# Optimization experiments

Measured on AMD Instinct MI355X. Metric: run time of the kernel, lower is better.

## Reference

```python
import jax, jax.numpy as jnp
import numpy as np

N_SRC = 50000
N_DST = 50000
N_EDGES = 600000
IN_FEAT = 128
OUT_FEAT = 128


def setup_inputs() -> dict:
    key = jax.random.key(0)
    k1, k2, k3, k4, k5, k6 = jax.random.split(key, 6)
    h_s = jax.random.normal(k1, (N_SRC, IN_FEAT), dtype=jnp.float32)
    h_d = jax.random.normal(k2, (N_DST, IN_FEAT), dtype=jnp.float32)
    src = jax.random.randint(k3, (N_EDGES,), 0, N_SRC, dtype=jnp.int32)
    dst = jax.random.randint(k4, (N_EDGES,), 0, N_DST, dtype=jnp.int32)
    # nn.Linear(in_feat*2, out_feat): W [out, 2*in], b [out]
    W = jax.random.normal(k5, (OUT_FEAT, 2 * IN_FEAT), dtype=jnp.float32) * 0.05
    b = jax.random.normal(k6, (OUT_FEAT,), dtype=jnp.float32) * 0.05
    return {"h_s": h_s, "h_d": h_d, "src": src, "dst": dst, "W": W, "b": b}


def reference(h_s, h_d, src, dst, W, b):
    # copy_u + mean: gather source features along edges, segment-mean by dst
    msgs = h_s[src]  # [E, in_feat]
    neigh_sum = jax.ops.segment_sum(msgs, dst, num_segments=N_DST)  # [n_dst, in_feat]
    deg = jax.ops.segment_sum(jnp.ones((src.shape[0],), dtype=h_s.dtype), dst,
                              num_segments=N_DST)
    h_neigh = neigh_sum / jnp.maximum(deg, 1.0)[:, None]  # zero-degree -> 0
    # concat + linear (dropout is identity in eval mode)
    feat = jnp.concatenate([h_d, h_neigh], axis=1)  # [n_dst, 2*in_feat]
    out = feat @ W.T + b  # [n_dst, out_feat]
    return out
```

## Files before the change

### kernel.cpp

```cpp
#include <hip/hip_runtime.h>
#include <hip/hip_bf16.h>

#define N_SRC 50000
#define N_DST 50000
#define N_EDGES 600000
#define IN_FEAT 128
#define OUT_FEAT 128
#define CAP 64

typedef __attribute__((ext_vector_type(8))) short short8;
typedef __attribute__((ext_vector_type(4))) float float4v;
typedef __attribute__((ext_vector_type(4))) float f32x4;

#define FILL_BLOCKS ((N_EDGES + 255) / 256)
#define HS4 (N_SRC * IN_FEAT / 4)
#define CVT_BLOCKS (HS4 / 256)
#define W_BLOCKS 16
#define K1_GRID (FILL_BLOCKS + 2 * CVT_BLOCKS + W_BLOCKS)

__global__ __launch_bounds__(256) void fill_cvt_kernel(
    const float* __restrict__ h_s, const float* __restrict__ h_d,
    const float* __restrict__ W,
    const int* __restrict__ src, const int* __restrict__ dst,
    int* __restrict__ deg, ushort* __restrict__ permu,
    ushort* __restrict__ hsb, ushort* __restrict__ hdb,
    ushort* __restrict__ wfrag)
{
    int bid = blockIdx.x;
    int tid = threadIdx.x;

    if (bid < FILL_BLOCKS) {
        int e = bid * 256 + tid;
        if (e < N_EDGES) {
            int s = __builtin_nontemporal_load(src + e);
            int d = __builtin_nontemporal_load(dst + e);
            int p = atomicAdd(&deg[d], 1);
            if (p < CAP) permu[(size_t)d * CAP + p] = (ushort)s;
        }
        return;
    }
    bid -= FILL_BLOCKS;

    if (bid < 2 * CVT_BLOCKS) {
        bool first = (bid < CVT_BLOCKS);
        const float* in = first ? h_s : h_d;
        ushort* outp    = first ? hsb : hdb;
        int idx = (first ? bid : bid - CVT_BLOCKS) * 256 + tid;
        f32x4 v = __builtin_nontemporal_load((const f32x4*)in + idx);
        __hip_bfloat16 o[4];
        o[0] = __float2bfloat16(v.x);
        o[1] = __float2bfloat16(v.y);
        o[2] = __float2bfloat16(v.z);
        o[3] = __float2bfloat16(v.w);
        *(ushort4*)(outp + (size_t)idx * 4) = *(ushort4*)o;
        return;
    }
    bid -= 2 * CVT_BLOCKS;

    int c = bid * 256 + tid;
    int f  = c >> 6;
    int l  = c & 63;
    int ks = f >> 3;
    int nt = f & 7;
    int row = nt * 16 + (l & 15);
    int col = ks * 32 + (l >> 4) * 8;
    const float* wp = W + (size_t)row * 256 + col;
    f32x4 w0 = __builtin_nontemporal_load((const f32x4*)wp);
    f32x4 w1 = __builtin_nontemporal_load((const f32x4*)wp + 1);
    __hip_bfloat16 o[8];
    o[0] = __float2bfloat16(w0.x); o[1] = __float2bfloat16(w0.y);
    o[2] = __float2bfloat16(w0.z); o[3] = __float2bfloat16(w0.w);
    o[4] = __float2bfloat16(w1.x); o[5] = __float2bfloat16(w1.y);
    o[6] = __float2bfloat16(w1.z); o[7] = __float2bfloat16(w1.w);
    *(short8*)(wfrag + (size_t)c * 8) = *(short8*)o;
}

__global__ __launch_bounds__(256) void gather_kernel(
    const ushort* __restrict__ hsb, const int* __restrict__ deg,
    const ushort* __restrict__ permu, ushort* __restrict__ neighb)
{
    int wave = threadIdx.x >> 6;
    int lane = threadIdx.x & 63;
    int row  = blockIdx.x * 4 + wave;
    if (row >= N_DST) return;

    int dg  = deg[row];
    int dgr = (dg < CAP) ? dg : CAP;
    const ushort* prow = permu + (size_t)row * CAP;
    int s0 = (dgr > 0) ? (int)prow[0] : 0;

    float ax = 0.f, ay = 0.f;
    for (int j = 0; j < dgr; j += 8) {
        ushort4 pa = *(const ushort4*)(prow + j);
        ushort4 pb = *(const ushort4*)(prow + j + 4);
        int t[8] = {pa.x, pa.y, pa.z, pa.w, pb.x, pb.y, pb.z, pb.w};
        int   s[8];
        float m[8];
#pragma unroll
        for (int q = 0; q < 8; ++q) {
            bool ok = (j + q < dgr);
            s[q] = ok ? t[q] : s0;
            m[q] = ok ? 1.f : 0.f;
        }
        ushort2 u[8];
#pragma unroll
        for (int q = 0; q < 8; ++q)
            u[q] = ((const ushort2*)(hsb + (size_t)s[q] * IN_FEAT))[lane];
#pragma unroll
        for (int q = 0; q < 8; ++q) {
            ax += m[q] * __uint_as_float((unsigned)u[q].x << 16);
            ay += m[q] * __uint_as_float((unsigned)u[q].y << 16);
        }
    }
    float inv = (dg > 0) ? (1.0f / (float)dg) : 0.0f;
    __hip_bfloat16 ox = __float2bfloat16(ax * inv);
    __hip_bfloat16 oy = __float2bfloat16(ay * inv);
    ushort2 o = make_ushort2(*(ushort*)&ox, *(ushort*)&oy);
    ((ushort2*)(neighb + (size_t)row * IN_FEAT))[lane] = o;
}

__global__ __launch_bounds__(256) void gemm_mfma_kernel(
    const ushort* __restrict__ hdb, const ushort* __restrict__ neighb,
    const ushort* __restrict__ wfrag, const float* __restrict__ b,
    float* __restrict__ out)
{
    __shared__ ushort sWb[64 * 64 * 8];

    int tid  = threadIdx.x;
    int wave = tid >> 6;
    int lane = tid & 63;
    int lm   = lane & 15;
    int lk   = (lane >> 4) * 8;

#pragma unroll
    for (int i = 0; i < 16; ++i) {
        int c = i * 256 + tid;
        *(short8*)(sWb + (size_t)c * 8) = *(const short8*)(wfrag + (size_t)c * 8);
    }
    __syncthreads();

    int row0 = blockIdx.x * 128 + wave * 32;

    float4v acc0[8], acc1[8];
#pragma unroll
    for (int nt = 0; nt < 8; ++nt) {
        acc0[nt] = (float4v){0.f, 0.f, 0.f, 0.f};
        acc1[nt] = (float4v){0.f, 0.f, 0.f, 0.f};
    }

    int ar0 = row0 + lm;       ar0 = (ar0 < N_DST) ? ar0 : (N_DST - 1);
    int ar1 = row0 + 16 + lm;  ar1 = (ar1 < N_DST) ? ar1 : (N_DST - 1);
    const ushort* a0h = hdb    + (size_t)ar0 * IN_FEAT + lk;
    const ushort* a1h = hdb    + (size_t)ar1 * IN_FEAT + lk;
    const ushort* a0n = neighb + (size_t)ar0 * IN_FEAT + lk;
    const ushort* a1n = neighb + (size_t)ar1 * IN_FEAT + lk;

#pragma unroll
    for (int ks = 0; ks < 8; ++ks) {
        int koff = (ks & 3) * 32;
        short8 af0 = (ks < 4) ? *(const short8*)(a0h + koff)
                              : *(const short8*)(a0n + koff);
        short8 af1 = (ks < 4) ? *(const short8*)(a1h + koff)
                              : *(const short8*)(a1n + koff);
#pragma unroll
        for (int nt = 0; nt < 8; ++nt) {
            short8 bf = *(const short8*)(sWb + ((size_t)(ks * 8 + nt) * 64 + lane) * 8);
            acc0[nt] = __builtin_amdgcn_mfma_f32_16x16x32_bf16(af0, bf, acc0[nt], 0, 0, 0);
            acc1[nt] = __builtin_amdgcn_mfma_f32_16x16x32_bf16(af1, bf, acc1[nt], 0, 0, 0);
        }
    }

    int orow0 = row0 + (lane >> 4) * 4;
#pragma unroll
    for (int nt = 0; nt < 8; ++nt) {
        int col = nt * 16 + lm;
        float bias = b[col];
#pragma unroll
        for (int r = 0; r < 4; ++r) {
            int oa = orow0 + r;
            int ob = oa + 16;
            if (oa < N_DST) out[(size_t)oa * OUT_FEAT + col] = acc0[nt][r] + bias;
            if (ob < N_DST) out[(size_t)ob * OUT_FEAT + col] = acc1[nt][r] + bias;
        }
    }
}

extern "C" void kernel_launch(void* const* d_in, const int* in_sizes, int n_in,
                              void* d_out, int out_size, void* d_ws, size_t ws_size,
                              hipStream_t stream) {
    const float* h_s = (const float*)d_in[0];
    const float* h_d = (const float*)d_in[1];
    const int*   src = (const int*)d_in[2];
    const int*   dst = (const int*)d_in[3];
    const float* W   = (const float*)d_in[4];
    const float* b   = (const float*)d_in[5];
    float* out = (float*)d_out;

    char* ws = (char*)d_ws;
    int*    deg    = (int*)ws;
    ushort* permu  = (ushort*)(ws + 200000);
    ushort* hsb    = (ushort*)(ws + 6600000);
    ushort* hdb    = (ushort*)(ws + 19400000);
    ushort* neighb = (ushort*)(ws + 32200000);
    ushort* wfrag  = (ushort*)(ws + 45000000);

    hipMemsetAsync(deg, 0, N_DST * sizeof(int), stream);

    fill_cvt_kernel<<<K1_GRID, 256, 0, stream>>>(
        h_s, h_d, W, src, dst, deg, permu, hsb, hdb, wfrag);
    gather_kernel<<<(N_DST + 3) / 4, 256, 0, stream>>>(
        hsb, deg, permu, neighb);
    gemm_mfma_kernel<<<(N_DST + 127) / 128, 256, 0, stream>>>(
        hdb, neighb, wfrag, b, out);
}
```

Measured before the change: 180.0 us.

## Add nontemporal stores, unroll first gather batch, drop LDS staging in GEMM

Conversion, gather and GEMM outputs now use nontemporal stores, and GEMM activations use nontemporal loads. The gather kernel issues the first 16 neighbour loads unconditionally, with out-of-range entries pointing at row 0 and masked to zero, which exposes more memory-level parallelism for typical degrees. The GEMM drops its per-block shared-memory copy of W and reads fragments straight from global/L2. It also halves rows per wave, doubling the grid so more blocks run concurrently. In exchange, the GEMM does more redundant W reads from cache, and nontemporal stores may evict data the next kernel wants to reuse.

Result: no change. 178.8 us (-0.6%).

```diff
diff --git a/kernel.cpp b/kernel.cpp
--- a/kernel.cpp
+++ b/kernel.cpp
@@ -11,6 +11,7 @@
 typedef __attribute__((ext_vector_type(8))) short short8;
 typedef __attribute__((ext_vector_type(4))) float float4v;
 typedef __attribute__((ext_vector_type(4))) float f32x4;
+typedef __attribute__((ext_vector_type(4))) unsigned short ushort4v;
 
 #define FILL_BLOCKS ((N_EDGES + 255) / 256)
 #define HS4 (N_SRC * IN_FEAT / 4)
@@ -52,7 +53,7 @@
         o[1] = __float2bfloat16(v.y);
         o[2] = __float2bfloat16(v.z);
         o[3] = __float2bfloat16(v.w);
-        *(ushort4*)(outp + (size_t)idx * 4) = *(ushort4*)o;
+        __builtin_nontemporal_store(*(ushort4v*)o, (ushort4v*)(outp + (size_t)idx * 4));
         return;
     }
     bid -= 2 * CVT_BLOCKS;
@@ -72,7 +73,7 @@
     o[2] = __float2bfloat16(w0.z); o[3] = __float2bfloat16(w0.w);
     o[4] = __float2bfloat16(w1.x); o[5] = __float2bfloat16(w1.y);
     o[6] = __float2bfloat16(w1.z); o[7] = __float2bfloat16(w1.w);
-    *(short8*)(wfrag + (size_t)c * 8) = *(short8*)o;
+    __builtin_nontemporal_store(*(short8*)o, (short8*)(wfrag + (size_t)c * 8));
 }
 
 __global__ __launch_bounds__(256) void gather_kernel(
@@ -87,36 +88,50 @@
     int dg  = deg[row];
     int dgr = (dg < CAP) ? dg : CAP;
     const ushort* prow = permu + (size_t)row * CAP;
-    int s0 = (dgr > 0) ? (int)prow[0] : 0;
 
     float ax = 0.f, ay = 0.f;
-    for (int j = 0; j < dgr; j += 8) {
+    {
+        ushort4 p0 = *(const ushort4*)(prow);
+        ushort4 p1 = *(const ushort4*)(prow + 4);
+        ushort4 p2 = *(const ushort4*)(prow + 8);
+        ushort4 p3 = *(const ushort4*)(prow + 12);
+        int t[16] = {p0.x, p0.y, p0.z, p0.w, p1.x, p1.y, p1.z, p1.w,
+                     p2.x, p2.y, p2.z, p2.w, p3.x, p3.y, p3.z, p3.w};
+        ushort2 u[16];
+#pragma unroll
+        for (int q = 0; q < 16; ++q) {
+            int s = (q < dgr) ? t[q] : 0;
+            u[q] = ((const ushort2*)(hsb + (size_t)s * IN_FEAT))[lane];
+        }
+#pragma unroll
+        for (int q = 0; q < 16; ++q) {
+            float m = (q < dgr) ? 1.f : 0.f;
+            ax += m * __uint_as_float((unsigned)u[q].x << 16);
+            ay += m * __uint_as_float((unsigned)u[q].y << 16);
+        }
+    }
+    for (int j = 16; j < dgr; j += 8) {
         ushort4 pa = *(const ushort4*)(prow + j);
         ushort4 pb = *(const ushort4*)(prow + j + 4);
         int t[8] = {pa.x, pa.y, pa.z, pa.w, pb.x, pb.y, pb.z, pb.w};
-        int   s[8];
-        float m[8];
+        ushort2 u[8];
 #pragma unroll
         for (int q = 0; q < 8; ++q) {
-            bool ok = (j + q < dgr);
-            s[q] = ok ? t[q] : s0;
-            m[q] = ok ? 1.f : 0.f;
-        }
-        ushort2 u[8];
-#pragma unroll
-        for (int q = 0; q < 8; ++q)
-            u[q] = ((const ushort2*)(hsb + (size_t)s[q] * IN_FEAT))[lane];
+            int s = (j + q < dgr) ? t[q] : 0;
+            u[q] = ((const ushort2*)(hsb + (size_t)s * IN_FEAT))[lane];
+        }
 #pragma unroll
         for (int q = 0; q < 8; ++q) {
-            ax += m[q] * __uint_as_float((unsigned)u[q].x << 16);
-            ay += m[q] * __uint_as_float((unsigned)u[q].y << 16);
+            float m = (j + q < dgr) ? 1.f : 0.f;
+            ax += m * __uint_as_float((unsigned)u[q].x << 16);
+            ay += m * __uint_as_float((unsigned)u[q].y << 16);
         }
     }
     float inv = (dg > 0) ? (1.0f / (float)dg) : 0.0f;
     __hip_bfloat16 ox = __float2bfloat16(ax * inv);
     __hip_bfloat16 oy = __float2bfloat16(ay * inv);
-    ushort2 o = make_ushort2(*(ushort*)&ox, *(ushort*)&oy);
-    ((ushort2*)(neighb + (size_t)row * IN_FEAT))[lane] = o;
+    unsigned pk = (unsigned)*(ushort*)&ox | ((unsigned)*(ushort*)&oy << 16);
+    __builtin_nontemporal_store(pk, (unsigned*)(neighb + (size_t)row * IN_FEAT) + lane);
 }
 
 __global__ __launch_bounds__(256) void gemm_mfma_kernel(
@@ -124,63 +139,45 @@
     const ushort* __restrict__ wfrag, const float* __restrict__ b,
     float* __restrict__ out)
 {
-    __shared__ ushort sWb[64 * 64 * 8];
-
     int tid  = threadIdx.x;
     int wave = tid >> 6;
     int lane = tid & 63;
     int lm   = lane & 15;
-    int lk   = (lane >> 4) * 8;
-
-#pragma unroll
-    for (int i = 0; i < 16; ++i) {
-        int c = i * 256 + tid;
-        *(short8*)(sWb + (size_t)c * 8) = *(const short8*)(wfrag + (size_t)c * 8);
-    }
-    __syncthreads();
-
-    int row0 = blockIdx.x * 128 + wave * 32;
-
-    float4v acc0[8], acc1[8];
-#pragma unroll
-    for (int nt = 0; nt < 8; ++nt) {
-        acc0[nt] = (float4v){0.f, 0.f, 0.f, 0.f};
-        acc1[nt] = (float4v){0.f, 0.f, 0.f, 0.f};
-    }
-
-    int ar0 = row0 + lm;       ar0 = (ar0 < N_DST) ? ar0 : (N_DST - 1);
-    int ar1 = row0 + 16 + lm;  ar1 = (ar1 < N_DST) ? ar1 : (N_DST - 1);
-    const ushort* a0h = hdb    + (size_t)ar0 * IN_FEAT + lk;
-    const ushort* a1h = hdb    + (size_t)ar1 * IN_FEAT + lk;
-    const ushort* a0n = neighb + (size_t)ar0 * IN_FEAT + lk;
-    const ushort* a1n = neighb + (size_t)ar1 * IN_FEAT + lk;
+    int lq   = lane >> 4;
+
+    int row0 = blockIdx.x * 64 + wave * 16;
+    int ar   = row0 + lm;  ar = (ar < N_DST) ? ar : (N_DST - 1);
+    const ushort* ah = hdb    + (size_t)ar * IN_FEAT + lq * 8;
+    const ushort* an = neighb + (size_t)ar * IN_FEAT + lq * 8;
+
+    float4v acc[8];
+#pragma unroll
+    for (int nt = 0; nt < 8; ++nt) acc[nt] = (float4v){0.f, 0.f, 0.f, 0.f};
 
 #pragma unroll
     for (int ks = 0; ks < 8; ++ks) {
         int koff = (ks & 3) * 32;
-        short8 af0 = (ks < 4) ? *(const short8*)(a0h + koff)
-                              : *(const short8*)(a0n + koff);
-        short8 af1 = (ks < 4) ? *(const short8*)(a1h + koff)
-                              : *(const short8*)(a1n + koff);
+        short8 af = (ks < 4)
+            ? __builtin_nontemporal_load((const short8*)(ah + koff))
+            : __builtin_nontemporal_load((const short8*)(an + koff));
 #pragma unroll
         for (int nt = 0; nt < 8; ++nt) {
-            short8 bf = *(const short8*)(sWb + ((size_t)(ks * 8 + nt) * 64 + lane) * 8);
-            acc0[nt] = __builtin_amdgcn_mfma_f32_16x16x32_bf16(af0, bf, acc0[nt], 0, 0, 0);
-            acc1[nt] = __builtin_amdgcn_mfma_f32_16x16x32_bf16(af1, bf, acc1[nt], 0, 0, 0);
-        }
-    }
-
-    int orow0 = row0 + (lane >> 4) * 4;
+            short8 bf = *(const short8*)(wfrag + ((size_t)(ks * 8 + nt) * 64 + lane) * 8);
+            acc[nt] = __builtin_amdgcn_mfma_f32_16x16x32_bf16(af, bf, acc[nt], 0, 0, 0);
+        }
+    }
+
+    int orow0 = row0 + lq * 4;
 #pragma unroll
     for (int nt = 0; nt < 8; ++nt) {
         int col = nt * 16 + lm;
         float bias = b[col];
 #pragma unroll
         for (int r = 0; r < 4; ++r) {
-            int oa = orow0 + r;
-            int ob = oa + 16;
-            if (oa < N_DST) out[(size_t)oa * OUT_FEAT + col] = acc0[nt][r] + bias;
-            if (ob < N_DST) out[(size_t)ob * OUT_FEAT + col] = acc1[nt][r] + bias;
+            int o = orow0 + r;
+            if (o < N_DST)
+                __builtin_nontemporal_store(acc[nt][r] + bias,
+                                            out + (size_t)o * OUT_FEAT + col);
         }
     }
 }
@@ -210,6 +207,6 @@
         h_s, h_d, W, src, dst, deg, permu, hsb, hdb, wfrag);
     gather_kernel<<<(N_DST + 3) / 4, 256, 0, stream>>>(
         hsb, deg, permu, neighb);
-    gemm_mfma_kernel<<<(N_DST + 127) / 128, 256, 0, stream>>>(
+    gemm_mfma_kernel<<<(N_DST + 63) / 64, 256, 0, stream>>>(
         hdb, neighb, wfrag, b, out);
 }
```
